# Kernel tuning notes

Hardware: AMD Instinct MI355X
Metric: run time of the kernel (lower is better)

## Reference

```python
import jax, jax.numpy as jnp
import numpy as np

N, E = 100000, 1600000
DIN, DH, DOUT = 256, 128, 32


def _glorot(key, fan_in, fan_out):
    lim = np.sqrt(6.0 / (fan_in + fan_out)).astype(np.float32)
    return jax.random.uniform(key, (fan_in, fan_out), jnp.float32, -lim, lim)


def setup_inputs() -> dict:
    key = jax.random.key(0)
    k0, k1, k2, k3 = jax.random.split(key, 4)
    x = jax.random.normal(k0, (N, DIN), dtype=jnp.float32)
    edge_index = jax.random.randint(k1, (2, E), 0, N, dtype=jnp.int64)
    return {
        "x": x,
        "edge_index": edge_index,
        "W1": _glorot(k2, DIN, DH),
        "b1": jnp.zeros((DH,), jnp.float32),
        "W2": _glorot(k3, DH, DOUT),
        "b2": jnp.zeros((DOUT,), jnp.float32),
    }


def _gcn_conv(h_in, W, b, src, dst, deg_norm_src, deg_norm_dst, n):
    # PyG GCNConv: linear transform, then sym-normalized scatter-add, then bias.
    h = h_in @ W                                   # [N, F_out]
    msg = h[src] * (deg_norm_src * deg_norm_dst)[:, None]  # [E+N, F_out]
    agg = jax.ops.segment_sum(msg, dst, num_segments=n)    # [N, F_out]
    return agg + b


def reference(x, edge_index, W1, b1, W2, b2):
    n = x.shape[0]
    loops = jnp.arange(n, dtype=edge_index.dtype)  # self-loops (GCNConv default)
    src = jnp.concatenate([edge_index[0], loops])
    dst = jnp.concatenate([edge_index[1], loops])
    deg = jax.ops.segment_sum(jnp.ones(src.shape[0], x.dtype), dst, num_segments=n)
    dis = jnp.where(deg > 0, jax.lax.rsqrt(deg), 0.0)  # deg^{-1/2}
    ns, nd = dis[src], dis[dst]
    h = jax.nn.relu(_gcn_conv(x, W1, b1, src, dst, ns, nd, n))
    out = _gcn_conv(h, W2, b2, src, dst, ns, nd, n)
    return jax.nn.log_softmax(out, axis=1)
```

## Files before the change

### kernel.cpp

```cpp
#include <hip/hip_runtime.h>
#include <cstdint>

#define DIN 256
#define DH 128
#define DOUT 32
#define CE 4096
#define BSH 9
#define MAXW 12288

typedef short s16x8 __attribute__((ext_vector_type(8)));
typedef float f32x4 __attribute__((ext_vector_type(4)));

__device__ inline ushort f2bf(float f) {
    uint u = __float_as_uint(f);
    u += 0x7fff + ((u >> 16) & 1);
    return (ushort)(u >> 16);
}
__device__ inline float bf_lo(uint u) { return __uint_as_float(u << 16); }
__device__ inline float bf_hi(uint u) { return __uint_as_float(u & 0xffff0000u); }
__device__ inline uint packbf(float a, float b) {
    return (uint)f2bf(a) | ((uint)f2bf(b) << 16);
}


__global__ __launch_bounds__(256) void k_prep(const float* __restrict__ W1,
                                              ushort* __restrict__ w1tg) {
    int o = blockIdx.x * 1024 + threadIdx.x * 4;
    int c = o >> 8;
    int k = o & 255;
    ushort4 v;
    v.x = f2bf(W1[(size_t)(k + 0) * DH + c]);
    v.y = f2bf(W1[(size_t)(k + 1) * DH + c]);
    v.z = f2bf(W1[(size_t)(k + 2) * DH + c]);
    v.w = f2bf(W1[(size_t)(k + 3) * DH + c]);
    *(ushort4*)(w1tg + o) = v;
}


__global__ __launch_bounds__(256) void k_part(
    const int* __restrict__ src, const int* __restrict__ dst,
    int2* __restrict__ pairs, int* __restrict__ tbl, int* __restrict__ gctr,
    int e, int nbuck) {
    __shared__ int cnt[256];
    __shared__ int boffs[256];
    __shared__ int sh[256];
    __shared__ int sd[CE];
    __shared__ int ss[CE];
    int tid = threadIdx.x;
    if (blockIdx.x == 0 && tid == 0) *gctr = 0;
    long blkbase = (long)blockIdx.x * CE;
    int ecnt = min(CE, (int)(e - blkbase));

    cnt[tid] = 0;
    __syncthreads();

    int dreg[CE / 256];
    #pragma unroll
    for (int k = 0; k < CE / 256; ++k) {
        int i = k * 256 + tid;
        int d = -1;
        if (i < ecnt) {
            d = dst[blkbase + i];
            atomicAdd(&cnt[d >> BSH], 1);
        }
        dreg[k] = d;
    }
    __syncthreads();
    sh[tid] = cnt[tid];
    __syncthreads();
    for (int off = 1; off < 256; off <<= 1) {
        int x = (tid >= off) ? sh[tid - off] : 0;
        __syncthreads();
        if (tid >= off) sh[tid] += x;
        __syncthreads();
    }
    boffs[tid] = (tid == 0) ? 0 : sh[tid - 1];
    cnt[tid] = 0;
    __syncthreads();
    #pragma unroll
    for (int k = 0; k < CE / 256; ++k) {
        int i = k * 256 + tid;
        if (i < ecnt) {
            int d = dreg[k];
            int b = d >> BSH;
            int slot = boffs[b] + atomicAdd(&cnt[b], 1);
            sd[slot] = d;
            ss[slot] = src[blkbase + i];
        }
    }
    __syncthreads();
    for (int i = tid; i < ecnt; i += 256)
        pairs[blkbase + i] = make_int2(sd[i], ss[i]);
    if (tid < nbuck) tbl[blockIdx.x * (nbuck + 1) + tid] = boffs[tid];
    if (tid == 0)    tbl[blockIdx.x * (nbuck + 1) + nbuck] = ecnt;
}


__global__ __launch_bounds__(256) void k_build(
    const int2* __restrict__ pairs, const int* __restrict__ tbl,
    int* __restrict__ deg, int* __restrict__ offs, float* __restrict__ dis,
    int* __restrict__ adj, int* __restrict__ gctr,
    int nblk1, int nbuck, int n) {
    __shared__ int indeg[512];
    __shared__ int excl[512];
    __shared__ int sh[256];
    __shared__ int adjS[MAXW];
    __shared__ int baseSh, totSh;
    int tid = threadIdx.x;
    int b = blockIdx.x;
    int nodebase = b << BSH;

    indeg[tid] = 0;
    indeg[tid + 256] = 0;
    __syncthreads();

    for (int run = tid; run < nblk1; run += 256) {
        const int* trow = tbl + run * (nbuck + 1);
        int s0 = trow[b], s1 = trow[b + 1];
        long base = (long)run * CE;
        for (int k = s0; k < s1; ++k) {
            int d = pairs[base + k].x;
            atomicAdd(&indeg[d - nodebase], 1);
        }
    }
    __syncthreads();

    int a0 = indeg[tid * 2];
    int a1 = indeg[tid * 2 + 1];
    sh[tid] = a0 + a1;
    __syncthreads();
    for (int off = 1; off < 256; off <<= 1) {
        int x = (tid >= off) ? sh[tid - off] : 0;
        __syncthreads();
        if (tid >= off) sh[tid] += x;
        __syncthreads();
    }
    int e0 = (tid == 0) ? 0 : sh[tid - 1];
    excl[tid * 2] = e0;
    excl[tid * 2 + 1] = e0 + a0;
    if (tid == 255) {
        totSh = sh[255];
        baseSh = atomicAdd(gctr, sh[255]);
    }
    __syncthreads();
    int base = baseSh;
    int L = totSh;

    int i0 = nodebase + tid * 2;
    if (i0 < n) {
        deg[i0] = a0 + 1;
        offs[i0] = base + excl[tid * 2];
        dis[i0] = rsqrtf((float)(a0 + 1));
    }
    if (i0 + 1 < n) {
        deg[i0 + 1] = a1 + 1;
        offs[i0 + 1] = base + excl[tid * 2 + 1];
        dis[i0 + 1] = rsqrtf((float)(a1 + 1));
    }
    indeg[tid] = 0;
    indeg[tid + 256] = 0;
    __syncthreads();

    if (L <= MAXW) {
        for (int run = tid; run < nblk1; run += 256) {
            const int* trow = tbl + run * (nbuck + 1);
            int s0 = trow[b], s1 = trow[b + 1];
            long pb = (long)run * CE;
            for (int k = s0; k < s1; ++k) {
                int2 p = pairs[pb + k];
                int local = p.x - nodebase;
                int pos = excl[local] + atomicAdd(&indeg[local], 1);
                adjS[pos] = p.y;
            }
        }
        __syncthreads();
        for (int i = tid; i < L; i += 256) adj[base + i] = adjS[i];
    } else {
        for (int run = tid; run < nblk1; run += 256) {
            const int* trow = tbl + run * (nbuck + 1);
            int s0 = trow[b], s1 = trow[b + 1];
            long pb = (long)run * CE;
            for (int k = s0; k < s1; ++k) {
                int2 p = pairs[pb + k];
                int local = p.x - nodebase;
                int pos = base + excl[local] + atomicAdd(&indeg[local], 1);
                adj[pos] = p.y;
            }
        }
    }
}


__global__ __launch_bounds__(256) void k_gemm1(
    const float* __restrict__ x, const ushort* __restrict__ w1tg,
    const float* __restrict__ dis, ushort* __restrict__ hs, int n) {
    __shared__ union {
        ushort w1t[128][136];
        ushort cs[128][136];
    } u;
    __shared__ ushort xs[128][72];

    int tid = threadIdx.x;
    int row0 = blockIdx.x * 128;
    int lane = tid & 63;
    int w = tid >> 6;
    int wr0 = w * 32;
    int l15 = lane & 15;
    int koff = (lane >> 4) * 8;

    f32x4 acc[2][8];
    #pragma unroll
    for (int i = 0; i < 2; ++i)
        #pragma unroll
        for (int j = 0; j < 8; ++j)
            acc[i][j] = (f32x4){0.f, 0.f, 0.f, 0.f};

    for (int kh = 0; kh < 2; ++kh) {
        {
            int c = tid >> 1;
            int seg = (tid & 1) * 64;
            const uint4* gsrc = (const uint4*)(w1tg + (size_t)c * 256 + kh * 128 + seg);
            uint4* ldst = (uint4*)&u.w1t[c][seg];
            #pragma unroll
            for (int q = 0; q < 8; ++q) ldst[q] = gsrc[q];
        }
        for (int kc2 = 0; kc2 < 2; ++kc2) {
            {
                int r = tid >> 1;
                int half = (tid & 1) * 32;
                int rr = row0 + r; if (rr >= n) rr = n - 1;
                const float4* xr = (const float4*)(x + (size_t)rr * DIN + kh * 128 + kc2 * 64 + half);
                float4 v[8];
                #pragma unroll
                for (int q = 0; q < 8; ++q) v[q] = xr[q];
                #pragma unroll
                for (int q = 0; q < 8; ++q) {
                    ushort4 o;
                    o.x = f2bf(v[q].x); o.y = f2bf(v[q].y);
                    o.z = f2bf(v[q].z); o.w = f2bf(v[q].w);
                    *(ushort4*)&xs[r][half + q * 4] = o;
                }
            }
            __syncthreads();
            #pragma unroll
            for (int kk = 0; kk < 64; kk += 32) {
                s16x8 a0 = *(const s16x8*)&xs[wr0 + l15][kk + koff];
                s16x8 a1 = *(const s16x8*)&xs[wr0 + 16 + l15][kk + koff];
                int kl = kc2 * 64 + kk + koff;
                #pragma unroll
                for (int ct = 0; ct < 8; ++ct) {
                    s16x8 b = *(const s16x8*)&u.w1t[ct * 16 + l15][kl];
                    acc[0][ct] = __builtin_amdgcn_mfma_f32_16x16x32_bf16(a0, b, acc[0][ct], 0, 0, 0);
                    acc[1][ct] = __builtin_amdgcn_mfma_f32_16x16x32_bf16(a1, b, acc[1][ct], 0, 0, 0);
                }
            }
            __syncthreads();
        }
    }

    float dv[2][4];
    #pragma unroll
    for (int rt = 0; rt < 2; ++rt)
        #pragma unroll
        for (int r = 0; r < 4; ++r) {
            int rg = row0 + wr0 + rt * 16 + (lane >> 4) * 4 + r;
            if (rg >= n) rg = n - 1;
            dv[rt][r] = dis[rg];
        }
    #pragma unroll
    for (int rt = 0; rt < 2; ++rt)
        #pragma unroll
        for (int ct = 0; ct < 8; ++ct)
            #pragma unroll
            for (int r = 0; r < 4; ++r)
                u.cs[wr0 + rt * 16 + (lane >> 4) * 4 + r][ct * 16 + l15] = f2bf(acc[rt][ct][r] * dv[rt][r]);
    __syncthreads();
    {
        int r = tid >> 1;
        int half = (tid & 1) * 64;
        if (row0 + r < n) {
            uint4* dstp = (uint4*)(hs + (size_t)(row0 + r) * DH + half);
            const uint4* s = (const uint4*)&u.cs[r][half];
            #pragma unroll
            for (int q = 0; q < 8; ++q) dstp[q] = s[q];
        }
    }
}


__global__ __launch_bounds__(256) void k_agg1(
    const ushort* __restrict__ hs, const float* __restrict__ dis,
    const int* __restrict__ offs, const int* __restrict__ deg,
    const int* __restrict__ adj, const float* __restrict__ b1,
    ushort* __restrict__ h1, int n) {
    int node = blockIdx.x * 4 + (threadIdx.x >> 6);
    if (node >= n) return;
    int lane = threadIdx.x & 63;
    int r = lane >> 4;
    int j = lane & 15;

    const uint4* hu4 = (const uint4*)hs;
    int off = offs[node];
    int nsrc = deg[node];

    float a8[8] = {0.f, 0.f, 0.f, 0.f, 0.f, 0.f, 0.f, 0.f};
    int i = r;
    for (; i + 12 < nsrc; i += 16) {
        int s0 = (i == 0) ? node : adj[off + i - 1];
        int s1 = adj[off + i + 3];
        int s2 = adj[off + i + 7];
        int s3 = adj[off + i + 11];
        uint4 v0 = hu4[(size_t)s0 * 16 + j];
        uint4 v1 = hu4[(size_t)s1 * 16 + j];
        uint4 v2 = hu4[(size_t)s2 * 16 + j];
        uint4 v3 = hu4[(size_t)s3 * 16 + j];
        a8[0] += bf_lo(v0.x) + bf_lo(v1.x) + bf_lo(v2.x) + bf_lo(v3.x);
        a8[1] += bf_hi(v0.x) + bf_hi(v1.x) + bf_hi(v2.x) + bf_hi(v3.x);
        a8[2] += bf_lo(v0.y) + bf_lo(v1.y) + bf_lo(v2.y) + bf_lo(v3.y);
        a8[3] += bf_hi(v0.y) + bf_hi(v1.y) + bf_hi(v2.y) + bf_hi(v3.y);
        a8[4] += bf_lo(v0.z) + bf_lo(v1.z) + bf_lo(v2.z) + bf_lo(v3.z);
        a8[5] += bf_hi(v0.z) + bf_hi(v1.z) + bf_hi(v2.z) + bf_hi(v3.z);
        a8[6] += bf_lo(v0.w) + bf_lo(v1.w) + bf_lo(v2.w) + bf_lo(v3.w);
        a8[7] += bf_hi(v0.w) + bf_hi(v1.w) + bf_hi(v2.w) + bf_hi(v3.w);
    }
    for (; i + 4 < nsrc; i += 8) {
        int s0 = (i == 0) ? node : adj[off + i - 1];
        int s1 = adj[off + i + 3];
        uint4 v0 = hu4[(size_t)s0 * 16 + j];
        uint4 v1 = hu4[(size_t)s1 * 16 + j];
        a8[0] += bf_lo(v0.x) + bf_lo(v1.x); a8[1] += bf_hi(v0.x) + bf_hi(v1.x);
        a8[2] += bf_lo(v0.y) + bf_lo(v1.y); a8[3] += bf_hi(v0.y) + bf_hi(v1.y);
        a8[4] += bf_lo(v0.z) + bf_lo(v1.z); a8[5] += bf_hi(v0.z) + bf_hi(v1.z);
        a8[6] += bf_lo(v0.w) + bf_lo(v1.w); a8[7] += bf_hi(v0.w) + bf_hi(v1.w);
    }
    if (i < nsrc) {
        int s0 = (i == 0) ? node : adj[off + i - 1];
        uint4 v0 = hu4[(size_t)s0 * 16 + j];
        a8[0] += bf_lo(v0.x); a8[1] += bf_hi(v0.x);
        a8[2] += bf_lo(v0.y); a8[3] += bf_hi(v0.y);
        a8[4] += bf_lo(v0.z); a8[5] += bf_hi(v0.z);
        a8[6] += bf_lo(v0.w); a8[7] += bf_hi(v0.w);
    }
    #pragma unroll
    for (int q = 0; q < 8; ++q) {
        a8[q] += __shfl_xor(a8[q], 16);
        a8[q] += __shfl_xor(a8[q], 32);
    }

    float dv = dis[node];
    float4 ba = ((const float4*)b1)[j * 2];
    float4 bb = ((const float4*)b1)[j * 2 + 1];
    if (r == 0) {
        uint4 ov;
        ov.x = packbf(fmaxf(a8[0] * dv + ba.x, 0.f), fmaxf(a8[1] * dv + ba.y, 0.f));
        ov.y = packbf(fmaxf(a8[2] * dv + ba.z, 0.f), fmaxf(a8[3] * dv + ba.w, 0.f));
        ov.z = packbf(fmaxf(a8[4] * dv + bb.x, 0.f), fmaxf(a8[5] * dv + bb.y, 0.f));
        ov.w = packbf(fmaxf(a8[6] * dv + bb.z, 0.f), fmaxf(a8[7] * dv + bb.w, 0.f));
        ((uint4*)h1)[(size_t)node * 16 + j] = ov;
    }
}


__global__ __launch_bounds__(256) void k_gemm2(
    const ushort* __restrict__ h1, const float* __restrict__ W2,
    const float* __restrict__ dis, ushort* __restrict__ h2s, int n) {
    int t = blockIdx.x * blockDim.x + threadIdx.x;
    int row = t >> 3;
    int cg = t & 7;
    if (row >= n) return;
    const uint2* hr = (const uint2*)(h1 + (size_t)row * DH);
    const float4* w4 = (const float4*)W2;
    float4 acc = make_float4(0.f, 0.f, 0.f, 0.f);
    #pragma unroll 8
    for (int k4 = 0; k4 < DH / 4; ++k4) {
        uint2 au = hr[k4];
        float a0 = bf_lo(au.x), a1 = bf_hi(au.x), a2 = bf_lo(au.y), a3 = bf_hi(au.y);
        float4 w0 = w4[(k4 * 4 + 0) * 8 + cg];
        float4 w1 = w4[(k4 * 4 + 1) * 8 + cg];
        float4 w2 = w4[(k4 * 4 + 2) * 8 + cg];
        float4 w3 = w4[(k4 * 4 + 3) * 8 + cg];
        acc.x += a0 * w0.x + a1 * w1.x + a2 * w2.x + a3 * w3.x;
        acc.y += a0 * w0.y + a1 * w1.y + a2 * w2.y + a3 * w3.y;
        acc.z += a0 * w0.z + a1 * w1.z + a2 * w2.z + a3 * w3.z;
        acc.w += a0 * w0.w + a1 * w1.w + a2 * w2.w + a3 * w3.w;
    }
    float dv = dis[row];
    ushort4 o;
    o.x = f2bf(acc.x * dv); o.y = f2bf(acc.y * dv);
    o.z = f2bf(acc.z * dv); o.w = f2bf(acc.w * dv);
    *(ushort4*)(h2s + (size_t)row * DOUT + cg * 4) = o;
}


__global__ __launch_bounds__(256) void k_agg2_lsm(
    const ushort* __restrict__ h2s, const float* __restrict__ dis,
    const int* __restrict__ offs, const int* __restrict__ deg,
    const int* __restrict__ adj, const float* __restrict__ b2,
    float* __restrict__ out, int n) {
    int node = blockIdx.x * 8 + (threadIdx.x >> 5);
    if (node >= n) return;
    int t32 = threadIdx.x & 31;
    int rr = t32 >> 2;
    int j = t32 & 3;

    const uint4* hu4 = (const uint4*)h2s;
    int off = offs[node];
    int nsrc = deg[node];

    float a8[8] = {0.f, 0.f, 0.f, 0.f, 0.f, 0.f, 0.f, 0.f};
    int i = rr;
    for (; i + 8 < nsrc; i += 16) {
        int s0 = (i == 0) ? node : adj[off + i - 1];
        int s1 = adj[off + i + 7];
        uint4 v0 = hu4[(size_t)s0 * 4 + j];
        uint4 v1 = hu4[(size_t)s1 * 4 + j];
        a8[0] += bf_lo(v0.x) + bf_lo(v1.x); a8[1] += bf_hi(v0.x) + bf_hi(v1.x);
        a8[2] += bf_lo(v0.y) + bf_lo(v1.y); a8[3] += bf_hi(v0.y) + bf_hi(v1.y);
        a8[4] += bf_lo(v0.z) + bf_lo(v1.z); a8[5] += bf_hi(v0.z) + bf_hi(v1.z);
        a8[6] += bf_lo(v0.w) + bf_lo(v1.w); a8[7] += bf_hi(v0.w) + bf_hi(v1.w);
    }
    if (i < nsrc) {
        int s0 = (i == 0) ? node : adj[off + i - 1];
        uint4 v0 = hu4[(size_t)s0 * 4 + j];
        a8[0] += bf_lo(v0.x); a8[1] += bf_hi(v0.x);
        a8[2] += bf_lo(v0.y); a8[3] += bf_hi(v0.y);
        a8[4] += bf_lo(v0.z); a8[5] += bf_hi(v0.z);
        a8[6] += bf_lo(v0.w); a8[7] += bf_hi(v0.w);
    }
    #pragma unroll
    for (int q = 0; q < 8; ++q) {
        a8[q] += __shfl_xor(a8[q], 4);
        a8[q] += __shfl_xor(a8[q], 8);
        a8[q] += __shfl_xor(a8[q], 16);
    }
    float dv = dis[node];
    float4 ba = ((const float4*)b2)[j * 2];
    float4 bb = ((const float4*)b2)[j * 2 + 1];
    float v[8];
    v[0] = a8[0] * dv + ba.x; v[1] = a8[1] * dv + ba.y;
    v[2] = a8[2] * dv + ba.z; v[3] = a8[3] * dv + ba.w;
    v[4] = a8[4] * dv + bb.x; v[5] = a8[5] * dv + bb.y;
    v[6] = a8[6] * dv + bb.z; v[7] = a8[7] * dv + bb.w;
    float m = v[0];
    #pragma unroll
    for (int q = 1; q < 8; ++q) m = fmaxf(m, v[q]);
    m = fmaxf(m, __shfl_xor(m, 1));
    m = fmaxf(m, __shfl_xor(m, 2));
    float s = 0.f;
    #pragma unroll
    for (int q = 0; q < 8; ++q) s += __expf(v[q] - m);
    s += __shfl_xor(s, 1);
    s += __shfl_xor(s, 2);
    float ls = m + __logf(s);
    if (rr == 0) {
        float4 o0 = make_float4(v[0] - ls, v[1] - ls, v[2] - ls, v[3] - ls);
        float4 o1 = make_float4(v[4] - ls, v[5] - ls, v[6] - ls, v[7] - ls);
        float* op = out + (size_t)node * DOUT + j * 8;
        *(float4*)op = o0;
        *(float4*)(op + 4) = o1;
    }
}

extern "C" void kernel_launch(void* const* d_in, const int* in_sizes, int n_in,
                              void* d_out, int out_size, void* d_ws, size_t ws_size,
                              hipStream_t stream) {
    const float* x  = (const float*)d_in[0];
    const int*   ei = (const int*)d_in[1];
    const float* W1 = (const float*)d_in[2];
    const float* b1 = (const float*)d_in[3];
    const float* W2 = (const float*)d_in[4];
    const float* b2 = (const float*)d_in[5];
    int n = in_sizes[0] / DIN;
    int e = in_sizes[1] / 2;
    const int* src = ei;
    const int* dst = ei + e;
    float* out = (float*)d_out;

    int nblk1 = (e + CE - 1) / CE;
    int nbuck = (n + 511) >> BSH;

    char* p = (char*)d_ws;
    int2*   pairs  = (int2*)p;    p += (size_t)e * 8;
    int*    tbl    = (int*)p;     p += (size_t)nblk1 * (nbuck + 1) * 4;
    int*    deg    = (int*)p;     p += (size_t)n * 4;
    int*    offs   = (int*)p;     p += (size_t)n * 4;
    int*    gctr   = (int*)p;     p += 1024;
    float*  dis    = (float*)p;   p += (size_t)n * 4;
    int*    adj    = (int*)p;     p += (size_t)e * 4;
    ushort* w1tg   = (ushort*)p;  p += (size_t)DIN * DH * 2;
    ushort* hs     = (ushort*)p;  p += (size_t)n * DH * 2;
    ushort* h1     = (ushort*)p;  p += (size_t)n * DH * 2;
    ushort* h2s    = (ushort*)p;

    k_prep<<<32, 256, 0, stream>>>(W1, w1tg);
    k_part<<<nblk1, 256, 0, stream>>>(src, dst, pairs, tbl, gctr, e, nbuck);
    k_build<<<nbuck, 256, 0, stream>>>(pairs, tbl, deg, offs, dis, adj, gctr,
                                       nblk1, nbuck, n);

    k_gemm1<<<(n + 127) / 128, 256, 0, stream>>>(x, w1tg, dis, hs, n);
    k_agg1<<<(n + 3) / 4, 256, 0, stream>>>(hs, dis, offs, deg, adj, b1, h1, n);
    k_gemm2<<<(n * 8 + 255) / 256, 256, 0, stream>>>(h1, W2, dis, h2s, n);
    k_agg2_lsm<<<(n + 7) / 8, 256, 0, stream>>>(h2s, dis, offs, deg, adj, b2, out, n);
}
```

Measured before the change: 275.5 us.

## Fuse layer-1 aggregation with layer-2 GEMM and pack edge pairs into 32 bits

Merges the first aggregation kernel and the second small GEMM into one kernel. Each block walks 64 nodes, keeps bf16 W2 in registers, and reduces the projection with shuffles. This removes the h1 round-trip through global memory and one launch. Separately, each (dst-local, src) edge pair is packed into one 32-bit word, halving partition traffic. The packing assumes node ids fit in 17 bits, and W2 is now rounded to bf16, which adds precision loss.

```diff
diff --git a/kernel.cpp b/kernel.cpp
--- a/kernel.cpp
+++ b/kernel.cpp
@@ -7,6 +7,7 @@
 #define CE 4096
 #define BSH 9
 #define MAXW 12288
+#define NPB 64
 
 typedef short s16x8 __attribute__((ext_vector_type(8)));
 typedef float f32x4 __attribute__((ext_vector_type(4)));
@@ -24,28 +25,41 @@
 
 
 __global__ __launch_bounds__(256) void k_prep(const float* __restrict__ W1,
-                                              ushort* __restrict__ w1tg) {
-    int o = blockIdx.x * 1024 + threadIdx.x * 4;
-    int c = o >> 8;
-    int k = o & 255;
-    ushort4 v;
-    v.x = f2bf(W1[(size_t)(k + 0) * DH + c]);
-    v.y = f2bf(W1[(size_t)(k + 1) * DH + c]);
-    v.z = f2bf(W1[(size_t)(k + 2) * DH + c]);
-    v.w = f2bf(W1[(size_t)(k + 3) * DH + c]);
-    *(ushort4*)(w1tg + o) = v;
+                                              ushort* __restrict__ w1tg,
+                                              const float* __restrict__ W2,
+                                              ushort* __restrict__ w2b) {
+    if (blockIdx.x < 32) {
+        int o = blockIdx.x * 1024 + threadIdx.x * 4;
+        int c = o >> 8;
+        int k = o & 255;
+        ushort4 v;
+        v.x = f2bf(W1[(size_t)(k + 0) * DH + c]);
+        v.y = f2bf(W1[(size_t)(k + 1) * DH + c]);
+        v.z = f2bf(W1[(size_t)(k + 2) * DH + c]);
+        v.w = f2bf(W1[(size_t)(k + 3) * DH + c]);
+        *(ushort4*)(w1tg + o) = v;
+    } else {
+        #pragma unroll
+        for (int q = 0; q < 4; ++q) {
+            int i4 = threadIdx.x + q * 256;
+            float4 v = ((const float4*)W2)[i4];
+            ushort4 o4;
+            o4.x = f2bf(v.x); o4.y = f2bf(v.y);
+            o4.z = f2bf(v.z); o4.w = f2bf(v.w);
+            *(ushort4*)(w2b + i4 * 4) = o4;
+        }
+    }
 }
 
 
 __global__ __launch_bounds__(256) void k_part(
     const int* __restrict__ src, const int* __restrict__ dst,
-    int2* __restrict__ pairs, int* __restrict__ tbl, int* __restrict__ gctr,
+    uint* __restrict__ pairs, int* __restrict__ tbl, int* __restrict__ gctr,
     int e, int nbuck) {
     __shared__ int cnt[256];
     __shared__ int boffs[256];
     __shared__ int sh[256];
-    __shared__ int sd[CE];
-    __shared__ int ss[CE];
+    __shared__ uint ps[CE];
     int tid = threadIdx.x;
     if (blockIdx.x == 0 && tid == 0) *gctr = 0;
     long blkbase = (long)blockIdx.x * CE;
@@ -84,20 +98,19 @@
             int d = dreg[k];
             int b = d >> BSH;
             int slot = boffs[b] + atomicAdd(&cnt[b], 1);
-            sd[slot] = d;
-            ss[slot] = src[blkbase + i];
+            ps[slot] = ((uint)(d & 511) << 17) | (uint)src[blkbase + i];
         }
     }
     __syncthreads();
     for (int i = tid; i < ecnt; i += 256)
-        pairs[blkbase + i] = make_int2(sd[i], ss[i]);
+        pairs[blkbase + i] = ps[i];
     if (tid < nbuck) tbl[blockIdx.x * (nbuck + 1) + tid] = boffs[tid];
     if (tid == 0)    tbl[blockIdx.x * (nbuck + 1) + nbuck] = ecnt;
 }
 
 
 __global__ __launch_bounds__(256) void k_build(
-    const int2* __restrict__ pairs, const int* __restrict__ tbl,
+    const uint* __restrict__ pairs, const int* __restrict__ tbl,
     int* __restrict__ deg, int* __restrict__ offs, float* __restrict__ dis,
     int* __restrict__ adj, int* __restrict__ gctr,
     int nblk1, int nbuck, int n) {
@@ -119,8 +132,8 @@
         int s0 = trow[b], s1 = trow[b + 1];
         long base = (long)run * CE;
         for (int k = s0; k < s1; ++k) {
-            int d = pairs[base + k].x;
-            atomicAdd(&indeg[d - nodebase], 1);
+            uint pp = pairs[base + k];
+            atomicAdd(&indeg[pp >> 17], 1);
         }
     }
     __syncthreads();
@@ -167,10 +180,10 @@
             int s0 = trow[b], s1 = trow[b + 1];
             long pb = (long)run * CE;
             for (int k = s0; k < s1; ++k) {
-                int2 p = pairs[pb + k];
-                int local = p.x - nodebase;
+                uint pp = pairs[pb + k];
+                int local = pp >> 17;
                 int pos = excl[local] + atomicAdd(&indeg[local], 1);
-                adjS[pos] = p.y;
+                adjS[pos] = (int)(pp & 0x1FFFFu);
             }
         }
         __syncthreads();
@@ -181,10 +194,10 @@
             int s0 = trow[b], s1 = trow[b + 1];
             long pb = (long)run * CE;
             for (int k = s0; k < s1; ++k) {
-                int2 p = pairs[pb + k];
-                int local = p.x - nodebase;
+                uint pp = pairs[pb + k];
+                int local = pp >> 17;
                 int pos = base + excl[local] + atomicAdd(&indeg[local], 1);
-                adj[pos] = p.y;
+                adj[pos] = (int)(pp & 0x1FFFFu);
             }
         }
     }
@@ -288,107 +301,110 @@
 }
 
 
-__global__ __launch_bounds__(256) void k_agg1(
+__global__ __launch_bounds__(256) void k_agg1g2(
     const ushort* __restrict__ hs, const float* __restrict__ dis,
     const int* __restrict__ offs, const int* __restrict__ deg,
     const int* __restrict__ adj, const float* __restrict__ b1,
-    ushort* __restrict__ h1, int n) {
-    int node = blockIdx.x * 4 + (threadIdx.x >> 6);
-    if (node >= n) return;
+    const ushort* __restrict__ w2b, ushort* __restrict__ h2s, int n) {
     int lane = threadIdx.x & 63;
+    int wv = threadIdx.x >> 6;
     int r = lane >> 4;
     int j = lane & 15;
 
-    const uint4* hu4 = (const uint4*)hs;
-    int off = offs[node];
-    int nsrc = deg[node];
-
-    float a8[8] = {0.f, 0.f, 0.f, 0.f, 0.f, 0.f, 0.f, 0.f};
-    int i = r;
-    for (; i + 12 < nsrc; i += 16) {
-        int s0 = (i == 0) ? node : adj[off + i - 1];
-        int s1 = adj[off + i + 3];
-        int s2 = adj[off + i + 7];
-        int s3 = adj[off + i + 11];
-        uint4 v0 = hu4[(size_t)s0 * 16 + j];
-        uint4 v1 = hu4[(size_t)s1 * 16 + j];
-        uint4 v2 = hu4[(size_t)s2 * 16 + j];
-        uint4 v3 = hu4[(size_t)s3 * 16 + j];
-        a8[0] += bf_lo(v0.x) + bf_lo(v1.x) + bf_lo(v2.x) + bf_lo(v3.x);
-        a8[1] += bf_hi(v0.x) + bf_hi(v1.x) + bf_hi(v2.x) + bf_hi(v3.x);
-        a8[2] += bf_lo(v0.y) + bf_lo(v1.y) + bf_lo(v2.y) + bf_lo(v3.y);
-        a8[3] += bf_hi(v0.y) + bf_hi(v1.y) + bf_hi(v2.y) + bf_hi(v3.y);
-        a8[4] += bf_lo(v0.z) + bf_lo(v1.z) + bf_lo(v2.z) + bf_lo(v3.z);
-        a8[5] += bf_hi(v0.z) + bf_hi(v1.z) + bf_hi(v2.z) + bf_hi(v3.z);
-        a8[6] += bf_lo(v0.w) + bf_lo(v1.w) + bf_lo(v2.w) + bf_lo(v3.w);
-        a8[7] += bf_hi(v0.w) + bf_hi(v1.w) + bf_hi(v2.w) + bf_hi(v3.w);
-    }
-    for (; i + 4 < nsrc; i += 8) {
-        int s0 = (i == 0) ? node : adj[off + i - 1];
-        int s1 = adj[off + i + 3];
-        uint4 v0 = hu4[(size_t)s0 * 16 + j];
-        uint4 v1 = hu4[(size_t)s1 * 16 + j];
-        a8[0] += bf_lo(v0.x) + bf_lo(v1.x); a8[1] += bf_hi(v0.x) + bf_hi(v1.x);
-        a8[2] += bf_lo(v0.y) + bf_lo(v1.y); a8[3] += bf_hi(v0.y) + bf_hi(v1.y);
-        a8[4] += bf_lo(v0.z) + bf_lo(v1.z); a8[5] += bf_hi(v0.z) + bf_hi(v1.z);
-        a8[6] += bf_lo(v0.w) + bf_lo(v1.w); a8[7] += bf_hi(v0.w) + bf_hi(v1.w);
-    }
-    if (i < nsrc) {
-        int s0 = (i == 0) ? node : adj[off + i - 1];
-        uint4 v0 = hu4[(size_t)s0 * 16 + j];
-        a8[0] += bf_lo(v0.x); a8[1] += bf_hi(v0.x);
-        a8[2] += bf_lo(v0.y); a8[3] += bf_hi(v0.y);
-        a8[4] += bf_lo(v0.z); a8[5] += bf_hi(v0.z);
-        a8[6] += bf_lo(v0.w); a8[7] += bf_hi(v0.w);
-    }
-    #pragma unroll
-    for (int q = 0; q < 8; ++q) {
-        a8[q] += __shfl_xor(a8[q], 16);
-        a8[q] += __shfl_xor(a8[q], 32);
-    }
-
-    float dv = dis[node];
+    uint4 w2u[8];
+    #pragma unroll
+    for (int kk = 0; kk < 8; ++kk)
+        w2u[kk] = *(const uint4*)(w2b + (size_t)(j * 8 + kk) * 32 + r * 8);
     float4 ba = ((const float4*)b1)[j * 2];
     float4 bb = ((const float4*)b1)[j * 2 + 1];
-    if (r == 0) {
-        uint4 ov;
-        ov.x = packbf(fmaxf(a8[0] * dv + ba.x, 0.f), fmaxf(a8[1] * dv + ba.y, 0.f));
-        ov.y = packbf(fmaxf(a8[2] * dv + ba.z, 0.f), fmaxf(a8[3] * dv + ba.w, 0.f));
-        ov.z = packbf(fmaxf(a8[4] * dv + bb.x, 0.f), fmaxf(a8[5] * dv + bb.y, 0.f));
-        ov.w = packbf(fmaxf(a8[6] * dv + bb.z, 0.f), fmaxf(a8[7] * dv + bb.w, 0.f));
-        ((uint4*)h1)[(size_t)node * 16 + j] = ov;
-    }
-}
-
-
-__global__ __launch_bounds__(256) void k_gemm2(
-    const ushort* __restrict__ h1, const float* __restrict__ W2,
-    const float* __restrict__ dis, ushort* __restrict__ h2s, int n) {
-    int t = blockIdx.x * blockDim.x + threadIdx.x;
-    int row = t >> 3;
-    int cg = t & 7;
-    if (row >= n) return;
-    const uint2* hr = (const uint2*)(h1 + (size_t)row * DH);
-    const float4* w4 = (const float4*)W2;
-    float4 acc = make_float4(0.f, 0.f, 0.f, 0.f);
-    #pragma unroll 8
-    for (int k4 = 0; k4 < DH / 4; ++k4) {
-        uint2 au = hr[k4];
-        float a0 = bf_lo(au.x), a1 = bf_hi(au.x), a2 = bf_lo(au.y), a3 = bf_hi(au.y);
-        float4 w0 = w4[(k4 * 4 + 0) * 8 + cg];
-        float4 w1 = w4[(k4 * 4 + 1) * 8 + cg];
-        float4 w2 = w4[(k4 * 4 + 2) * 8 + cg];
-        float4 w3 = w4[(k4 * 4 + 3) * 8 + cg];
-        acc.x += a0 * w0.x + a1 * w1.x + a2 * w2.x + a3 * w3.x;
-        acc.y += a0 * w0.y + a1 * w1.y + a2 * w2.y + a3 * w3.y;
-        acc.z += a0 * w0.z + a1 * w1.z + a2 * w2.z + a3 * w3.z;
-        acc.w += a0 * w0.w + a1 * w1.w + a2 * w2.w + a3 * w3.w;
-    }
-    float dv = dis[row];
-    ushort4 o;
-    o.x = f2bf(acc.x * dv); o.y = f2bf(acc.y * dv);
-    o.z = f2bf(acc.z * dv); o.w = f2bf(acc.w * dv);
-    *(ushort4*)(h2s + (size_t)row * DOUT + cg * 4) = o;
+
+    const uint4* hu4 = (const uint4*)hs;
+    int nend = min(blockIdx.x * NPB + NPB, n);
+    for (int node = blockIdx.x * NPB + wv; node < nend; node += 4) {
+        int off = offs[node];
+        int nsrc = deg[node];
+
+        float a8[8] = {0.f, 0.f, 0.f, 0.f, 0.f, 0.f, 0.f, 0.f};
+        int i = r;
+        for (; i + 12 < nsrc; i += 16) {
+            int s0 = (i == 0) ? node : adj[off + i - 1];
+            int s1 = adj[off + i + 3];
+            int s2 = adj[off + i + 7];
+            int s3 = adj[off + i + 11];
+            uint4 v0 = hu4[(size_t)s0 * 16 + j];
+            uint4 v1 = hu4[(size_t)s1 * 16 + j];
+            uint4 v2 = hu4[(size_t)s2 * 16 + j];
+            uint4 v3 = hu4[(size_t)s3 * 16 + j];
+            a8[0] += bf_lo(v0.x) + bf_lo(v1.x) + bf_lo(v2.x) + bf_lo(v3.x);
+            a8[1] += bf_hi(v0.x) + bf_hi(v1.x) + bf_hi(v2.x) + bf_hi(v3.x);
+            a8[2] += bf_lo(v0.y) + bf_lo(v1.y) + bf_lo(v2.y) + bf_lo(v3.y);
+            a8[3] += bf_hi(v0.y) + bf_hi(v1.y) + bf_hi(v2.y) + bf_hi(v3.y);
+            a8[4] += bf_lo(v0.z) + bf_lo(v1.z) + bf_lo(v2.z) + bf_lo(v3.z);
+            a8[5] += bf_hi(v0.z) + bf_hi(v1.z) + bf_hi(v2.z) + bf_hi(v3.z);
+            a8[6] += bf_lo(v0.w) + bf_lo(v1.w) + bf_lo(v2.w) + bf_lo(v3.w);
+            a8[7] += bf_hi(v0.w) + bf_hi(v1.w) + bf_hi(v2.w) + bf_hi(v3.w);
+        }
+        for (; i + 4 < nsrc; i += 8) {
+            int s0 = (i == 0) ? node : adj[off + i - 1];
+            int s1 = adj[off + i + 3];
+            uint4 v0 = hu4[(size_t)s0 * 16 + j];
+            uint4 v1 = hu4[(size_t)s1 * 16 + j];
+            a8[0] += bf_lo(v0.x) + bf_lo(v1.x); a8[1] += bf_hi(v0.x) + bf_hi(v1.x);
+            a8[2] += bf_lo(v0.y) + bf_lo(v1.y); a8[3] += bf_hi(v0.y) + bf_hi(v1.y);
+            a8[4] += bf_lo(v0.z) + bf_lo(v1.z); a8[5] += bf_hi(v0.z) + bf_hi(v1.z);
+            a8[6] += bf_lo(v0.w) + bf_lo(v1.w); a8[7] += bf_hi(v0.w) + bf_hi(v1.w);
+        }
+        if (i < nsrc) {
+            int s0 = (i == 0) ? node : adj[off + i - 1];
+            uint4 v0 = hu4[(size_t)s0 * 16 + j];
+            a8[0] += bf_lo(v0.x); a8[1] += bf_hi(v0.x);
+            a8[2] += bf_lo(v0.y); a8[3] += bf_hi(v0.y);
+            a8[4] += bf_lo(v0.z); a8[5] += bf_hi(v0.z);
+            a8[6] += bf_lo(v0.w); a8[7] += bf_hi(v0.w);
+        }
+        #pragma unroll
+        for (int q = 0; q < 8; ++q) {
+            a8[q] += __shfl_xor(a8[q], 16);
+            a8[q] += __shfl_xor(a8[q], 32);
+        }
+
+        float dv = dis[node];
+        float h1v[8];
+        h1v[0] = fmaxf(a8[0] * dv + ba.x, 0.f);
+        h1v[1] = fmaxf(a8[1] * dv + ba.y, 0.f);
+        h1v[2] = fmaxf(a8[2] * dv + ba.z, 0.f);
+        h1v[3] = fmaxf(a8[3] * dv + ba.w, 0.f);
+        h1v[4] = fmaxf(a8[4] * dv + bb.x, 0.f);
+        h1v[5] = fmaxf(a8[5] * dv + bb.y, 0.f);
+        h1v[6] = fmaxf(a8[6] * dv + bb.z, 0.f);
+        h1v[7] = fmaxf(a8[7] * dv + bb.w, 0.f);
+
+        float p[8] = {0.f, 0.f, 0.f, 0.f, 0.f, 0.f, 0.f, 0.f};
+        #pragma unroll
+        for (int kk = 0; kk < 8; ++kk) {
+            float hv = h1v[kk];
+            uint4 wv4 = w2u[kk];
+            p[0] += hv * bf_lo(wv4.x); p[1] += hv * bf_hi(wv4.x);
+            p[2] += hv * bf_lo(wv4.y); p[3] += hv * bf_hi(wv4.y);
+            p[4] += hv * bf_lo(wv4.z); p[5] += hv * bf_hi(wv4.z);
+            p[6] += hv * bf_lo(wv4.w); p[7] += hv * bf_hi(wv4.w);
+        }
+        #pragma unroll
+        for (int oo = 0; oo < 8; ++oo) {
+            p[oo] += __shfl_xor(p[oo], 1);
+            p[oo] += __shfl_xor(p[oo], 2);
+            p[oo] += __shfl_xor(p[oo], 4);
+            p[oo] += __shfl_xor(p[oo], 8);
+        }
+        if (j == 0) {
+            uint4 ov;
+            ov.x = packbf(p[0] * dv, p[1] * dv);
+            ov.y = packbf(p[2] * dv, p[3] * dv);
+            ov.z = packbf(p[4] * dv, p[5] * dv);
+            ov.w = packbf(p[6] * dv, p[7] * dv);
+            *(uint4*)(h2s + (size_t)node * DOUT + r * 8) = ov;
+        }
+    }
 }
 
 
@@ -480,7 +496,7 @@
     int nbuck = (n + 511) >> BSH;
 
     char* p = (char*)d_ws;
-    int2*   pairs  = (int2*)p;    p += (size_t)e * 8;
+    uint*   pairs  = (uint*)p;    p += (size_t)e * 4;
     int*    tbl    = (int*)p;     p += (size_t)nblk1 * (nbuck + 1) * 4;
     int*    deg    = (int*)p;     p += (size_t)n * 4;
     int*    offs   = (int*)p;     p += (size_t)n * 4;
@@ -488,17 +504,17 @@
     float*  dis    = (float*)p;   p += (size_t)n * 4;
     int*    adj    = (int*)p;     p += (size_t)e * 4;
     ushort* w1tg   = (ushort*)p;  p += (size_t)DIN * DH * 2;
+    ushort* w2b    = (ushort*)p;  p += (size_t)DH * DOUT * 2;
     ushort* hs     = (ushort*)p;  p += (size_t)n * DH * 2;
-    ushort* h1     = (ushort*)p;  p += (size_t)n * DH * 2;
     ushort* h2s    = (ushort*)p;
 
-    k_prep<<<32, 256, 0, stream>>>(W1, w1tg);
+    k_prep<<<33, 256, 0, stream>>>(W1, w1tg, W2, w2b);
     k_part<<<nblk1, 256, 0, stream>>>(src, dst, pairs, tbl, gctr, e, nbuck);
     k_build<<<nbuck, 256, 0, stream>>>(pairs, tbl, deg, offs, dis, adj, gctr,
                                        nblk1, nbuck, n);
 
     k_gemm1<<<(n + 127) / 128, 256, 0, stream>>>(x, w1tg, dis, hs, n);
-    k_agg1<<<(n + 3) / 4, 256, 0, stream>>>(hs, dis, offs, deg, adj, b1, h1, n);
-    k_gemm2<<<(n * 8 + 255) / 256, 256, 0, stream>>>(h1, W2, dis, h2s, n);
+    k_agg1g2<<<(n + NPB - 1) / NPB, 256, 0, stream>>>(hs, dis, offs, deg, adj,
+                                                      b1, w2b, h2s, n);
     k_agg2_lsm<<<(n + 7) / 8, 256, 0, stream>>>(h2s, dis, offs, deg, adj, b2, out, n);
 }
```

New measurement: 277.9 us. Within noise of the previous version (+0.9%).

## Quantize layer-1 features to int8 with per-row scales and pack edge pairs

Applied to the files above, without the earlier changes.

The layer-1 transformed features are stored as unsigned 8-bit values with a per-row float scale instead of bf16, which halves the bytes gathered per neighbor in the first aggregation. An offset correction term is subtracted from the sums to undo the +128 bias. Separately, edge partition pairs are packed into one 32-bit word (9-bit local destination, 17-bit source), halving that intermediate traffic. The risk is accuracy loss from int8 quantization, and the packing assumes node ids below 131072.

```diff
diff --git a/kernel.cpp b/kernel.cpp
--- a/kernel.cpp
+++ b/kernel.cpp
@@ -21,6 +21,10 @@
 __device__ inline uint packbf(float a, float b) {
     return (uint)f2bf(a) | ((uint)f2bf(b) << 16);
 }
+__device__ inline float ub0(uint v) { return (float)(v & 0xFFu); }
+__device__ inline float ub1(uint v) { return (float)((v >> 8) & 0xFFu); }
+__device__ inline float ub2(uint v) { return (float)((v >> 16) & 0xFFu); }
+__device__ inline float ub3(uint v) { return (float)(v >> 24); }
 
 
 __global__ __launch_bounds__(256) void k_prep(const float* __restrict__ W1,
@@ -39,13 +43,12 @@
 
 __global__ __launch_bounds__(256) void k_part(
     const int* __restrict__ src, const int* __restrict__ dst,
-    int2* __restrict__ pairs, int* __restrict__ tbl, int* __restrict__ gctr,
+    uint* __restrict__ pairs, int* __restrict__ tbl, int* __restrict__ gctr,
     int e, int nbuck) {
     __shared__ int cnt[256];
     __shared__ int boffs[256];
     __shared__ int sh[256];
-    __shared__ int sd[CE];
-    __shared__ int ss[CE];
+    __shared__ uint ps[CE];
     int tid = threadIdx.x;
     if (blockIdx.x == 0 && tid == 0) *gctr = 0;
     long blkbase = (long)blockIdx.x * CE;
@@ -84,20 +87,19 @@
             int d = dreg[k];
             int b = d >> BSH;
             int slot = boffs[b] + atomicAdd(&cnt[b], 1);
-            sd[slot] = d;
-            ss[slot] = src[blkbase + i];
+            ps[slot] = ((uint)(d & 511) << 17) | (uint)src[blkbase + i];
         }
     }
     __syncthreads();
     for (int i = tid; i < ecnt; i += 256)
-        pairs[blkbase + i] = make_int2(sd[i], ss[i]);
+        pairs[blkbase + i] = ps[i];
     if (tid < nbuck) tbl[blockIdx.x * (nbuck + 1) + tid] = boffs[tid];
     if (tid == 0)    tbl[blockIdx.x * (nbuck + 1) + nbuck] = ecnt;
 }
 
 
 __global__ __launch_bounds__(256) void k_build(
-    const int2* __restrict__ pairs, const int* __restrict__ tbl,
+    const uint* __restrict__ pairs, const int* __restrict__ tbl,
     int* __restrict__ deg, int* __restrict__ offs, float* __restrict__ dis,
     int* __restrict__ adj, int* __restrict__ gctr,
     int nblk1, int nbuck, int n) {
@@ -119,8 +121,8 @@
         int s0 = trow[b], s1 = trow[b + 1];
         long base = (long)run * CE;
         for (int k = s0; k < s1; ++k) {
-            int d = pairs[base + k].x;
-            atomicAdd(&indeg[d - nodebase], 1);
+            uint pp = pairs[base + k];
+            atomicAdd(&indeg[pp >> 17], 1);
         }
     }
     __syncthreads();
@@ -167,10 +169,10 @@
             int s0 = trow[b], s1 = trow[b + 1];
             long pb = (long)run * CE;
             for (int k = s0; k < s1; ++k) {
-                int2 p = pairs[pb + k];
-                int local = p.x - nodebase;
+                uint pp = pairs[pb + k];
+                int local = pp >> 17;
                 int pos = excl[local] + atomicAdd(&indeg[local], 1);
-                adjS[pos] = p.y;
+                adjS[pos] = (int)(pp & 0x1FFFFu);
             }
         }
         __syncthreads();
@@ -181,10 +183,10 @@
             int s0 = trow[b], s1 = trow[b + 1];
             long pb = (long)run * CE;
             for (int k = s0; k < s1; ++k) {
-                int2 p = pairs[pb + k];
-                int local = p.x - nodebase;
+                uint pp = pairs[pb + k];
+                int local = pp >> 17;
                 int pos = base + excl[local] + atomicAdd(&indeg[local], 1);
-                adj[pos] = p.y;
+                adj[pos] = (int)(pp & 0x1FFFFu);
             }
         }
     }
@@ -193,10 +195,11 @@
 
 __global__ __launch_bounds__(256) void k_gemm1(
     const float* __restrict__ x, const ushort* __restrict__ w1tg,
-    const float* __restrict__ dis, ushort* __restrict__ hs, int n) {
+    const float* __restrict__ dis, uchar* __restrict__ hs8,
+    float* __restrict__ scl, int n) {
     __shared__ union {
         ushort w1t[128][136];
-        ushort cs[128][136];
+        uchar  cs8[128][144];
     } u;
     __shared__ ushort xs[128][72];
 
@@ -268,84 +271,104 @@
             dv[rt][r] = dis[rg];
         }
     #pragma unroll
-    for (int rt = 0; rt < 2; ++rt)
+    for (int rt = 0; rt < 2; ++rt) {
         #pragma unroll
-        for (int ct = 0; ct < 8; ++ct)
+        for (int r = 0; r < 4; ++r) {
+            int lrow = wr0 + rt * 16 + (lane >> 4) * 4 + r;
+            float vals[8];
+            float mx = 0.f;
             #pragma unroll
-            for (int r = 0; r < 4; ++r)
-                u.cs[wr0 + rt * 16 + (lane >> 4) * 4 + r][ct * 16 + l15] = f2bf(acc[rt][ct][r] * dv[rt][r]);
+            for (int ct = 0; ct < 8; ++ct) {
+                vals[ct] = acc[rt][ct][r] * dv[rt][r];
+                mx = fmaxf(mx, fabsf(vals[ct]));
+            }
+            mx = fmaxf(mx, __shfl_xor(mx, 1));
+            mx = fmaxf(mx, __shfl_xor(mx, 2));
+            mx = fmaxf(mx, __shfl_xor(mx, 4));
+            mx = fmaxf(mx, __shfl_xor(mx, 8));
+            float s = mx * (1.f / 127.f);
+            float inv = (mx > 0.f) ? 127.f / mx : 0.f;
+            #pragma unroll
+            for (int ct = 0; ct < 8; ++ct)
+                u.cs8[lrow][ct * 16 + l15] = (uchar)(__float2int_rn(vals[ct] * inv) + 128);
+            if (l15 == 0 && row0 + lrow < n) scl[row0 + lrow] = s;
+        }
+    }
     __syncthreads();
     {
         int r = tid >> 1;
         int half = (tid & 1) * 64;
         if (row0 + r < n) {
-            uint4* dstp = (uint4*)(hs + (size_t)(row0 + r) * DH + half);
-            const uint4* s = (const uint4*)&u.cs[r][half];
+            uint4* dstp = (uint4*)(hs8 + (size_t)(row0 + r) * 128 + half);
+            const uint4* sp = (const uint4*)&u.cs8[r][half];
             #pragma unroll
-            for (int q = 0; q < 8; ++q) dstp[q] = s[q];
+            for (int q = 0; q < 4; ++q) dstp[q] = sp[q];
         }
     }
 }
 
 
 __global__ __launch_bounds__(256) void k_agg1(
-    const ushort* __restrict__ hs, const float* __restrict__ dis,
-    const int* __restrict__ offs, const int* __restrict__ deg,
-    const int* __restrict__ adj, const float* __restrict__ b1,
-    ushort* __restrict__ h1, int n) {
+    const uchar* __restrict__ hs8, const float* __restrict__ scl,
+    const float* __restrict__ dis, const int* __restrict__ offs,
+    const int* __restrict__ deg, const int* __restrict__ adj,
+    const float* __restrict__ b1, ushort* __restrict__ h1, int n) {
     int node = blockIdx.x * 4 + (threadIdx.x >> 6);
     if (node >= n) return;
     int lane = threadIdx.x & 63;
     int r = lane >> 4;
     int j = lane & 15;
 
-    const uint4* hu4 = (const uint4*)hs;
+    const uint2* hq = (const uint2*)hs8;
     int off = offs[node];
     int nsrc = deg[node];
 
     float a8[8] = {0.f, 0.f, 0.f, 0.f, 0.f, 0.f, 0.f, 0.f};
+    float ss = 0.f;
     int i = r;
+    #define ACC8(v, c)                                      \
+        a8[0] += ub0((v).x) * (c); a8[1] += ub1((v).x) * (c); \
+        a8[2] += ub2((v).x) * (c); a8[3] += ub3((v).x) * (c); \
+        a8[4] += ub0((v).y) * (c); a8[5] += ub1((v).y) * (c); \
+        a8[6] += ub2((v).y) * (c); a8[7] += ub3((v).y) * (c); \
+        ss += (c);
     for (; i + 12 < nsrc; i += 16) {
         int s0 = (i == 0) ? node : adj[off + i - 1];
         int s1 = adj[off + i + 3];
         int s2 = adj[off + i + 7];
         int s3 = adj[off + i + 11];
-        uint4 v0 = hu4[(size_t)s0 * 16 + j];
-        uint4 v1 = hu4[(size_t)s1 * 16 + j];
-        uint4 v2 = hu4[(size_t)s2 * 16 + j];
-        uint4 v3 = hu4[(size_t)s3 * 16 + j];
-        a8[0] += bf_lo(v0.x) + bf_lo(v1.x) + bf_lo(v2.x) + bf_lo(v3.x);
-        a8[1] += bf_hi(v0.x) + bf_hi(v1.x) + bf_hi(v2.x) + bf_hi(v3.x);
-        a8[2] += bf_lo(v0.y) + bf_lo(v1.y) + bf_lo(v2.y) + bf_lo(v3.y);
-        a8[3] += bf_hi(v0.y) + bf_hi(v1.y) + bf_hi(v2.y) + bf_hi(v3.y);
-        a8[4] += bf_lo(v0.z) + bf_lo(v1.z) + bf_lo(v2.z) + bf_lo(v3.z);
-        a8[5] += bf_hi(v0.z) + bf_hi(v1.z) + bf_hi(v2.z) + bf_hi(v3.z);
-        a8[6] += bf_lo(v0.w) + bf_lo(v1.w) + bf_lo(v2.w) + bf_lo(v3.w);
-        a8[7] += bf_hi(v0.w) + bf_hi(v1.w) + bf_hi(v2.w) + bf_hi(v3.w);
+        float c0 = scl[s0], c1 = scl[s1], c2 = scl[s2], c3 = scl[s3];
+        uint2 v0 = hq[(size_t)s0 * 16 + j];
+        uint2 v1 = hq[(size_t)s1 * 16 + j];
+        uint2 v2 = hq[(size_t)s2 * 16 + j];
+        uint2 v3 = hq[(size_t)s3 * 16 + j];
+        ACC8(v0, c0) ACC8(v1, c1) ACC8(v2, c2) ACC8(v3, c3)
     }
     for (; i + 4 < nsrc; i += 8) {
         int s0 = (i == 0) ? node : adj[off + i - 1];
         int s1 = adj[off + i + 3];
-        uint4 v0 = hu4[(size_t)s0 * 16 + j];
-        uint4 v1 = hu4[(size_t)s1 * 16 + j];
-        a8[0] += bf_lo(v0.x) + bf_lo(v1.x); a8[1] += bf_hi(v0.x) + bf_hi(v1.x);
-        a8[2] += bf_lo(v0.y) + bf_lo(v1.y); a8[3] += bf_hi(v0.y) + bf_hi(v1.y);
-        a8[4] += bf_lo(v0.z) + bf_lo(v1.z); a8[5] += bf_hi(v0.z) + bf_hi(v1.z);
-        a8[6] += bf_lo(v0.w) + bf_lo(v1.w); a8[7] += bf_hi(v0.w) + bf_hi(v1.w);
+        float c0 = scl[s0], c1 = scl[s1];
+        uint2 v0 = hq[(size_t)s0 * 16 + j];
+        uint2 v1 = hq[(size_t)s1 * 16 + j];
+        ACC8(v0, c0) ACC8(v1, c1)
     }
     if (i < nsrc) {
         int s0 = (i == 0) ? node : adj[off + i - 1];
-        uint4 v0 = hu4[(size_t)s0 * 16 + j];
-        a8[0] += bf_lo(v0.x); a8[1] += bf_hi(v0.x);
-        a8[2] += bf_lo(v0.y); a8[3] += bf_hi(v0.y);
-        a8[4] += bf_lo(v0.z); a8[5] += bf_hi(v0.z);
-        a8[6] += bf_lo(v0.w); a8[7] += bf_hi(v0.w);
-    }
+        float c0 = scl[s0];
+        uint2 v0 = hq[(size_t)s0 * 16 + j];
+        ACC8(v0, c0)
+    }
+    #undef ACC8
     #pragma unroll
     for (int q = 0; q < 8; ++q) {
         a8[q] += __shfl_xor(a8[q], 16);
         a8[q] += __shfl_xor(a8[q], 32);
     }
+    ss += __shfl_xor(ss, 16);
+    ss += __shfl_xor(ss, 32);
+    float corr = 128.f * ss;
+    #pragma unroll
+    for (int q = 0; q < 8; ++q) a8[q] -= corr;
 
     float dv = dis[node];
     float4 ba = ((const float4*)b1)[j * 2];
@@ -480,7 +503,7 @@
     int nbuck = (n + 511) >> BSH;
 
     char* p = (char*)d_ws;
-    int2*   pairs  = (int2*)p;    p += (size_t)e * 8;
+    uint*   pairs  = (uint*)p;    p += (size_t)e * 4;
     int*    tbl    = (int*)p;     p += (size_t)nblk1 * (nbuck + 1) * 4;
     int*    deg    = (int*)p;     p += (size_t)n * 4;
     int*    offs   = (int*)p;     p += (size_t)n * 4;
@@ -488,7 +511,8 @@
     float*  dis    = (float*)p;   p += (size_t)n * 4;
     int*    adj    = (int*)p;     p += (size_t)e * 4;
     ushort* w1tg   = (ushort*)p;  p += (size_t)DIN * DH * 2;
-    ushort* hs     = (ushort*)p;  p += (size_t)n * DH * 2;
+    uchar*  hs8    = (uchar*)p;   p += (size_t)n * DH;
+    float*  scl    = (float*)p;   p += (size_t)n * 4;
     ushort* h1     = (ushort*)p;  p += (size_t)n * DH * 2;
     ushort* h2s    = (ushort*)p;
 
@@ -497,8 +521,8 @@
     k_build<<<nbuck, 256, 0, stream>>>(pairs, tbl, deg, offs, dis, adj, gctr,
                                        nblk1, nbuck, n);
 
-    k_gemm1<<<(n + 127) / 128, 256, 0, stream>>>(x, w1tg, dis, hs, n);
-    k_agg1<<<(n + 3) / 4, 256, 0, stream>>>(hs, dis, offs, deg, adj, b1, h1, n);
+    k_gemm1<<<(n + 127) / 128, 256, 0, stream>>>(x, w1tg, dis, hs8, scl, n);
+    k_agg1<<<(n + 3) / 4, 256, 0, stream>>>(hs8, scl, dis, offs, deg, adj, b1, h1, n);
     k_gemm2<<<(n * 8 + 255) / 256, 256, 0, stream>>>(h1, W2, dis, h2s, n);
     k_agg2_lsm<<<(n + 7) / 8, 256, 0, stream>>>(h2s, dis, offs, deg, adj, b2, out, n);
 }
```

Measured after the change: 242.2 us. 12.1% less time.
